# Optimization experiments

Measured on AMD Instinct MI355X. Metric: run time of the kernel, lower is better.

## Reference

```python
import jax, jax.numpy as jnp
import numpy as np

C_IN = 512
OUT_CH = 256  # query/key gate channels
DIM = 64      # squeeze/extraction rank


def setup_inputs() -> dict:
    key = jax.random.key(0)
    ks = jax.random.split(key, 11)
    b, c, h, w = 16, C_IN, 64, 64

    def winit(k, o, i):
        # torch Conv2d default init: U(-s, s), s = 1/sqrt(fan_in)
        s = 1.0 / np.sqrt(i)
        return jax.random.uniform(k, (o, i), jnp.float32, -s, s)

    return {
        "x": jax.random.normal(ks[0], (b, c, h, w), jnp.float32),
        "Wq": winit(ks[1], OUT_CH, C_IN), "bq": winit(ks[2], OUT_CH, C_IN)[:, 0],
        "Wk": winit(ks[3], OUT_CH, C_IN), "bk": winit(ks[4], OUT_CH, C_IN)[:, 0],
        "Wv": winit(ks[5], C_IN, C_IN),   "bv": winit(ks[6], C_IN, C_IN)[:, 0],
        "Ws": winit(ks[7], DIM, C_IN),    "bs": winit(ks[8], DIM, C_IN)[:, 0],
        "We": winit(ks[9], DIM, C_IN),    "be": winit(ks[10], DIM, C_IN)[:, 0],
    }


def reference(x, Wq, bq, Wk, bk, Wv, bv, Ws, bs, We, be):
    b, c, h, w = x.shape
    n = h * w
    xf = x.reshape(b, c, n)  # [b, 512, n] (1x1 conv == matmul over channels)

    Q = jnp.einsum('oc,bcn->bon', Wq, xf) + bq[:, None]   # [b, 256, n]
    K = jnp.einsum('oc,bcn->bon', Wk, xf) + bk[:, None]   # [b, 256, n]
    gate = jax.nn.sigmoid(jnp.mean(Q * K, axis=1, keepdims=True))  # [b, 1, n]

    V = jnp.einsum('oc,bcn->bon', Wv, xf) + bv[:, None]   # [b, 512, n]
    V_dw = V * gate                                        # [b, 512, n]

    Qs = jnp.einsum('oc,bcn->bon', Ws, xf) + bs[:, None]   # [b, 64, n]
    Ke = jnp.einsum('oc,bcn->bon', We, xf) + be[:, None]   # [b, 64, n]

    energy = jnp.einsum('bcn,bdn->bcd', V_dw, Qs)           # [b, 512, 64]
    attention = jax.nn.softmax(energy, axis=-1)
    Vout = jnp.einsum('bcd,bdn->bcn', attention, Ke)        # [b, 512, n]

    return x + Vout.reshape(b, c, h, w)
```

## Files before the change

### kernel.cpp

```cpp
#include <hip/hip_runtime.h>

#define BATCH 16
#define CIN 512
#define NPIX 4096

typedef __attribute__((ext_vector_type(8))) short bf16x8;
typedef __attribute__((ext_vector_type(4))) float f32x4;

#define MFMA(a,b,c) __builtin_amdgcn_mfma_f32_16x16x32_bf16((a),(b),(c),0,0,0)

#define GLOAD(g, l) __builtin_amdgcn_global_load_lds( \
    (const __attribute__((address_space(1))) unsigned int*)(g), \
    (__attribute__((address_space(3))) unsigned int*)(l), 16, 0, 0)

union PK  { short s[8]; bf16x8 v; };
union PK4 { short s[4]; uint2 u; };

__device__ __forceinline__ unsigned short bf16_rne(float f){
  unsigned u = __float_as_uint(f);
  return (unsigned short)((u + 0x7fffu + ((u >> 16) & 1u)) >> 16);
}
__device__ __forceinline__ void f32_split(float f, short &h, short &l){
  unsigned short hu = bf16_rne(f);
  h = (short)hu;
  float fh = __uint_as_float((unsigned)hu << 16);
  l = (short)bf16_rne(f - fh);
}
__device__ __forceinline__ void split8(float4 a, float4 b, bf16x8 &h, bf16x8 &l){
  float vv[8] = {a.x,a.y,a.z,a.w,b.x,b.y,b.z,b.w};
  PK ph, pl;
  #pragma unroll
  for (int z=0;z<8;z++){ short hh,ll; f32_split(vv[z],hh,ll); ph.s[z]=hh; pl.s[z]=ll; }
  h = ph.v; l = pl.v;
}

__device__ __forceinline__ int offBig(int row, int k){
  int s = k >> 3;
  s = (s & ~7) | ((s ^ row) & 7);
  return row*512 + s*8 + (k & 7);
}

__global__ __launch_bounds__(256)
void k_convw(const float* __restrict__ Wq, const float* __restrict__ bq,
             const float* __restrict__ Wk, const float* __restrict__ bk,
             const float* __restrict__ Ws, const float* __restrict__ bs,
             const float* __restrict__ We, const float* __restrict__ be,
             short* __restrict__ WALL, short* __restrict__ WLOT,
             float* __restrict__ BG, float* __restrict__ BSE){
  int t = blockIdx.x*256 + threadIdx.x;
  if (t < 640*512){
    int r = t >> 9, k = t & 511;
    float v = (r < 512) ? ((r & 1) ? Wk[(r>>1)*512 + k] : Wq[(r>>1)*512 + k])
            : (r < 576) ? Ws[(r-512)*512 + k] : We[(r-576)*512 + k];
    short h, l; f32_split(v, h, l);
    int kt = k >> 5, lc = (k >> 3) & 3, e = k & 7;
    int pc = lc ^ (r & 3);
    WALL[((size_t)kt*640 + r)*32 + pc*8 + e] = h;
    if (r >= 512 && r < 576){
      int rlo = r - 512;
      WLOT[((size_t)kt*64 + rlo)*32 + (lc ^ (rlo & 3))*8 + e] = l;
    }
  }
  if (t < 512) BG[t] = (t & 1) ? bk[t>>1] : bq[t>>1];
  if (t < 128) BSE[t] = (t < 64) ? bs[t] : be[t-64];
}

__global__ __launch_bounds__(512, 2)
void k_front(const float* __restrict__ x, const short* __restrict__ WALL,
             const short* __restrict__ WLOT, const float* __restrict__ BG,
             const float* __restrict__ BSE,
             float* __restrict__ QSG, short* __restrict__ KET, float* __restrict__ S){
  __shared__ __align__(16) short AB[2][640*32];
  __shared__ __align__(16) short LO[2][64*32];
  __shared__ __align__(16) short XS[64*512];
  __shared__ float QKf[512];
  __shared__ float GF[64];
  int nt = blockIdx.x, b = blockIdx.y;
  int n0 = nt*64;
  int tid = threadIdx.x, w = tid>>6, lane = tid&63;
  int lr = lane&15, lk = (lane>>4)<<3;
  int cg = lane>>4;

  {
    const char* src = (const char*)WALL;
    #pragma unroll
    for (int i=0;i<5;i++){
      int slot = i*8 + w;
      GLOAD(src + slot*1024 + lane*16, ((char*)&AB[0][0]) + slot*1024);
    }
    if (w < 4)
      GLOAD((const char*)WLOT + w*1024 + lane*16, ((char*)&LO[0][0]) + w*1024);
  }

  {
    int cc0 = tid >> 2;
    int ni  = (tid & 3) * 4;
    #pragma unroll
    for (int p=0;p<4;p++){
      int cc = p*128 + cc0;
      const float* xp = x + ((size_t)b*CIN + cc)*NPIX + n0 + ni;
      float4 vv[4];
      #pragma unroll
      for (int u=0;u<4;u++) vv[u] = *(const float4*)(xp + u*16);
      #pragma unroll
      for (int u=0;u<4;u++){
        float f[4] = {vv[u].x, vv[u].y, vv[u].z, vv[u].w};
        #pragma unroll
        for (int z=0;z<4;z++)
          XS[offBig(ni + u*16 + z, cc)] = (short)bf16_rne(f[z]);
      }
    }
  }

  f32x4 acc[5][4] = {};
  int rowBase = w*80;

  for (int kt=0; kt<16; kt++){
    int cur = kt & 1;
    __syncthreads();
    if (kt < 15){
      const char* src = (const char*)WALL + (size_t)(kt+1)*40960;
      #pragma unroll
      for (int i=0;i<5;i++){
        int slot = i*8 + w;
        GLOAD(src + slot*1024 + lane*16, ((char*)&AB[cur^1][0]) + slot*1024);
      }
      if (w < 4)
        GLOAD((const char*)WLOT + (size_t)(kt+1)*4096 + w*1024 + lane*16,
              ((char*)&LO[cur^1][0]) + w*1024);
    }
    bf16x8 bb[4];
    #pragma unroll
    for (int j=0;j<4;j++)
      bb[j] = *(const bf16x8*)&XS[offBig(j*16+lr, kt*32+lk)];
    int swz = ((cg ^ (lr & 3)) << 3);
    #pragma unroll
    for (int r=0;r<5;r++){
      int rowL = rowBase + r*16 + lr;
      bf16x8 a = *(const bf16x8*)&AB[cur][rowL*32 + swz];
      #pragma unroll
      for (int j=0;j<4;j++) acc[r][j] = MFMA(a, bb[j], acc[r][j]);
      int F = w*5 + r;
      if (F >= 32 && F < 36){
        int rowLo = F*16 - 512 + lr;
        bf16x8 alo = *(const bf16x8*)&LO[cur][rowLo*32 + swz];
        #pragma unroll
        for (int j=0;j<4;j++) acc[r][j] = MFMA(alo, bb[j], acc[r][j]);
      }
    }
  }

  int rq = (lane>>4)<<2;
  {
    float p[4] = {0.f,0.f,0.f,0.f};
    #pragma unroll
    for (int r=0;r<5;r++){
      int F = w*5 + r;
      if (F < 32){
        f32x4 bg = *(const f32x4*)&BG[F*16 + rq];
        #pragma unroll
        for (int j=0;j<4;j++){
          f32x4 a4 = acc[r][j];
          p[j] += (a4[0]+bg[0])*(a4[1]+bg[1]) + (a4[2]+bg[2])*(a4[3]+bg[3]);
        }
      }
    }
    #pragma unroll
    for (int j=0;j<4;j++){ p[j] += __shfl_xor(p[j],16); p[j] += __shfl_xor(p[j],32); }
    if (lane < 16){
      #pragma unroll
      for (int j=0;j<4;j++) QKf[w*64 + j*16 + lane] = p[j];
    }
  }
  __syncthreads();
  if (tid < 64){
    float s = 0.f;
    #pragma unroll
    for (int ww=0;ww<8;ww++) s += QKf[ww*64 + tid];
    GF[tid] = 1.f/(1.f + __expf(-s*(1.f/256.f)));
  }
  __syncthreads();

  #pragma unroll
  for (int r=0;r<5;r++){
    int F = w*5 + r;
    if (F >= 32 && F < 36){
      int row0 = F*16 - 512 + rq;
      f32x4 bs4 = *(const f32x4*)&BSE[row0];
      float srow[4] = {0.f,0.f,0.f,0.f};
      #pragma unroll
      for (int j=0;j<4;j++){
        int nl = j*16 + lr;
        float g = GF[nl];
        int n = n0 + nl;
        #pragma unroll
        for (int q=0;q<4;q++){
          float v = (acc[r][j][q] + bs4[q]) * g;
          QSG[((size_t)(b*64) + row0 + q)*NPIX + n] = v;
          srow[q] += v;
        }
      }
      #pragma unroll
      for (int q=0;q<4;q++){
        float v = srow[q];
        v += __shfl_xor(v,1); v += __shfl_xor(v,2);
        v += __shfl_xor(v,4); v += __shfl_xor(v,8);
        if (lr == 0) atomicAdd(&S[b*64 + row0 + q], v);
      }
    } else if (F >= 36){
      int d0 = F*16 - 576 + rq;
      f32x4 be4 = *(const f32x4*)&BSE[64 + d0];
      #pragma unroll
      for (int j=0;j<4;j++){
        int n = n0 + j*16 + lr;
        PK4 pk;
        #pragma unroll
        for (int q=0;q<4;q++) pk.s[q] = (short)bf16_rne(acc[r][j][q] + be4[q]);
        *(uint2*)&KET[((size_t)(b*NPIX) + n)*64 + d0] = pk.u;
      }
    }
  }
}

__global__ __launch_bounds__(512)
void k_M(const float* __restrict__ x, const float* __restrict__ QSG,
         float* __restrict__ M){
  int slab = blockIdx.x, b = blockIdx.y;
  int tid = threadIdx.x, w = tid>>6, lane = tid&63;
  int lr = lane&15, lk8 = (lane>>4)<<3;
  f32x4 acc[4][4] = {};
  for (int kt=0; kt<8; kt++){
    int noff = slab*256 + kt*32 + lk8;
    bf16x8 bh[4], bl[4];
    #pragma unroll
    for (int j=0;j<4;j++){
      const float* qp = QSG + ((size_t)(b*64) + j*16 + lr)*NPIX + noff;
      split8(*(const float4*)qp, *(const float4*)(qp+4), bh[j], bl[j]);
    }
    #pragma unroll
    for (int r=0;r<4;r++){
      const float* xp = x + ((size_t)(b*CIN) + w*64 + r*16 + lr)*NPIX + noff;
      bf16x8 ah, al;
      split8(*(const float4*)xp, *(const float4*)(xp+4), ah, al);
      #pragma unroll
      for (int j=0;j<4;j++){
        acc[r][j] = MFMA(al, bh[j], acc[r][j]);
        acc[r][j] = MFMA(ah, bl[j], acc[r][j]);
        acc[r][j] = MFMA(ah, bh[j], acc[r][j]);
      }
    }
  }
  int rq = (lane>>4)<<2;
  #pragma unroll
  for (int r=0;r<4;r++)
    #pragma unroll
    for (int j=0;j<4;j++)
      #pragma unroll
      for (int q=0;q<4;q++)
        atomicAdd(&M[((size_t)(b*CIN) + w*64 + r*16 + rq + q)*64 + j*16 + lr], acc[r][j][q]);
}

__global__ __launch_bounds__(256)
void k_energy(const float* __restrict__ Wv, const float* __restrict__ bv,
              const float* __restrict__ M, const float* __restrict__ S,
              float* __restrict__ EN){
  __shared__ __align__(16) float ML[128*68];
  int cch = blockIdx.x, b = blockIdx.y;
  int tid = threadIdx.x;
  int d4 = tid & 15, ci = tid >> 4;
  f32x4 acc[2] = {};
  for (int kt=0; kt<4; kt++){
    __syncthreads();
    for (int i = tid; i < 2048; i += 256){
      int k = i >> 4, c4 = (i & 15) * 4;
      *(float4*)&ML[k*68 + c4] = *(const float4*)&M[((size_t)(b*CIN) + kt*128 + k)*64 + c4];
    }
    __syncthreads();
    #pragma unroll
    for (int m=0;m<2;m++){
      int c = cch*32 + ci + 16*m;
      const float* wvp = Wv + (size_t)c*512 + kt*128;
      for (int k4=0;k4<32;k4++){
        float4 wv4 = *(const float4*)(wvp + k4*4);
        f32x4 m0 = *(const f32x4*)&ML[(k4*4+0)*68 + d4*4];
        f32x4 m1 = *(const f32x4*)&ML[(k4*4+1)*68 + d4*4];
        f32x4 m2 = *(const f32x4*)&ML[(k4*4+2)*68 + d4*4];
        f32x4 m3 = *(const f32x4*)&ML[(k4*4+3)*68 + d4*4];
        acc[m] += m0*wv4.x + m1*wv4.y + m2*wv4.z + m3*wv4.w;
      }
    }
  }
  f32x4 s4 = *(const f32x4*)&S[b*64 + d4*4];
  #pragma unroll
  for (int m=0;m<2;m++){
    int c = cch*32 + ci + 16*m;
    f32x4 r = acc[m] + s4*bv[c];
    *(f32x4*)&EN[((size_t)(b*CIN) + c)*64 + d4*4] = r;
  }
}

__global__ __launch_bounds__(256)
void k_softmax(const float* __restrict__ EN, short* __restrict__ ATT){
  int row = blockIdx.x*4 + (threadIdx.x>>6);
  int lane = threadIdx.x & 63;
  float v = EN[(size_t)row*64 + lane];
  float m = v;
  #pragma unroll
  for (int s=1;s<64;s<<=1) m = fmaxf(m, __shfl_xor(m, s));
  float e = __expf(v - m);
  float sum = e;
  #pragma unroll
  for (int s=1;s<64;s<<=1) sum += __shfl_xor(sum, s);
  ATT[(size_t)row*64 + lane] = (short)bf16_rne(e / sum);
}

__global__ __launch_bounds__(512)
void k_out(const float* __restrict__ x, const short* __restrict__ ATT,
           const short* __restrict__ KET, float* __restrict__ out){
  int nt = blockIdx.x, b = blockIdx.y;
  int n0 = nt*64;
  int tid = threadIdx.x, w = tid>>6, lane = tid&63;
  int lr = lane&15, lk = (lane>>4)<<3;
  f32x4 acc[4][4] = {};
  #pragma unroll
  for (int kt=0; kt<2; kt++){
    bf16x8 bb[4];
    #pragma unroll
    for (int j=0;j<4;j++)
      bb[j] = *(const bf16x8*)&KET[((size_t)(b*NPIX) + n0 + j*16 + lr)*64 + kt*32 + lk];
    #pragma unroll
    for (int r=0;r<4;r++){
      bf16x8 a = *(const bf16x8*)&ATT[((size_t)(b*CIN) + w*64 + r*16 + lr)*64 + kt*32 + lk];
      #pragma unroll
      for (int j=0;j<4;j++)
        acc[r][j] = MFMA(a, bb[j], acc[r][j]);
    }
  }
  int rq = (lane>>4)<<2;
  #pragma unroll
  for (int r=0;r<4;r++)
    #pragma unroll
    for (int j=0;j<4;j++){
      int col = n0 + j*16 + lr;
      #pragma unroll
      for (int q=0;q<4;q++){
        size_t idx = ((size_t)(b*CIN) + w*64 + r*16 + rq + q)*NPIX + col;
        out[idx] = x[idx] + acc[r][j][q];
      }
    }
}

extern "C" void kernel_launch(void* const* d_in, const int* in_sizes, int n_in,
                              void* d_out, int out_size, void* d_ws, size_t ws_size,
                              hipStream_t stream){
  const float* x   = (const float*)d_in[0];
  const float* Wq  = (const float*)d_in[1];
  const float* bq  = (const float*)d_in[2];
  const float* Wk  = (const float*)d_in[3];
  const float* bk  = (const float*)d_in[4];
  const float* Wv  = (const float*)d_in[5];
  const float* bv  = (const float*)d_in[6];
  const float* Wsq = (const float*)d_in[7];
  const float* bsq = (const float*)d_in[8];
  const float* We  = (const float*)d_in[9];
  const float* be  = (const float*)d_in[10];
  float* out = (float*)d_out;

  char* wsb = (char*)d_ws;
  size_t off = 0;
  auto alloc = [&](size_t bytes)->void*{
    void* p = wsb + off; off += (bytes + 255) & ~(size_t)255; return p;
  };
  short* WALL = (short*)alloc((size_t)640*512*2);
  short* WLOT = (short*)alloc((size_t)64*512*2);
  float* BG   = (float*)alloc(512*4);
  float* BSE  = (float*)alloc(128*4);
  float* QSG  = (float*)alloc((size_t)BATCH*64*NPIX*4);
  short* KET  = (short*)alloc((size_t)BATCH*NPIX*64*2);
  float* Mb   = (float*)alloc((size_t)BATCH*512*64*4);
  float* Sb   = (float*)alloc((size_t)BATCH*64*4);
  float* EN   = (float*)alloc((size_t)BATCH*512*64*4);
  short* ATT  = (short*)alloc((size_t)BATCH*512*64*2);

  hipMemsetAsync(Mb, 0, (size_t)BATCH*512*64*4, stream);
  hipMemsetAsync(Sb, 0, (size_t)BATCH*64*4, stream);

  k_convw  <<<1280, 256, 0, stream>>>(Wq,bq,Wk,bk,Wsq,bsq,We,be, WALL,WLOT,BG,BSE);
  k_front  <<<dim3(64,16), 512, 0, stream>>>(x, WALL, WLOT, BG, BSE, QSG, KET, Sb);
  k_M      <<<dim3(16,16), 512, 0, stream>>>(x, QSG, Mb);
  k_energy <<<dim3(16,16), 256, 0, stream>>>(Wv, bv, Mb, Sb, EN);
  k_softmax<<<2048, 256, 0, stream>>>(EN, ATT);
  k_out    <<<dim3(64,16), 512, 0, stream>>>(x, ATT, KET, out);
}
```

Before: 276.0 us.

## Double k_front pixel tile and read weights straight from global memory

The front projection kernel now processes 128 pixels per block instead of 64, which halves the grid and doubles the per-wave accumulators to 5x8 MFMA tiles. This reuses each weight fragment across twice as many pixels. The double-buffered LDS staging of the weight tiles through global_load_lds is removed, and the A fragments are loaded directly from global memory each k-step. In exchange, weight-load latency is no longer hidden by prefetch, register pressure roughly doubles with a risk of spills, and the 128 KB activation tile in LDS limits the kernel to one block per CU.

```diff
diff --git a/kernel.cpp b/kernel.cpp
--- a/kernel.cpp
+++ b/kernel.cpp
@@ -8,10 +8,6 @@
 typedef __attribute__((ext_vector_type(4))) float f32x4;
 
 #define MFMA(a,b,c) __builtin_amdgcn_mfma_f32_16x16x32_bf16((a),(b),(c),0,0,0)
-
-#define GLOAD(g, l) __builtin_amdgcn_global_load_lds( \
-    (const __attribute__((address_space(1))) unsigned int*)(g), \
-    (__attribute__((address_space(3))) unsigned int*)(l), 16, 0, 0)
 
 union PK  { short s[8]; bf16x8 v; };
 union PK4 { short s[4]; uint2 u; };
@@ -70,40 +66,27 @@
              const short* __restrict__ WLOT, const float* __restrict__ BG,
              const float* __restrict__ BSE,
              float* __restrict__ QSG, short* __restrict__ KET, float* __restrict__ S){
-  __shared__ __align__(16) short AB[2][640*32];
-  __shared__ __align__(16) short LO[2][64*32];
-  __shared__ __align__(16) short XS[64*512];
-  __shared__ float QKf[512];
-  __shared__ float GF[64];
+  __shared__ __align__(16) short XS[128*512];
+  __shared__ float QKf[8*128];
+  __shared__ float GF[128];
   int nt = blockIdx.x, b = blockIdx.y;
-  int n0 = nt*64;
+  int n0 = nt*128;
   int tid = threadIdx.x, w = tid>>6, lane = tid&63;
   int lr = lane&15, lk = (lane>>4)<<3;
   int cg = lane>>4;
 
   {
-    const char* src = (const char*)WALL;
-    #pragma unroll
-    for (int i=0;i<5;i++){
-      int slot = i*8 + w;
-      GLOAD(src + slot*1024 + lane*16, ((char*)&AB[0][0]) + slot*1024);
-    }
-    if (w < 4)
-      GLOAD((const char*)WLOT + w*1024 + lane*16, ((char*)&LO[0][0]) + w*1024);
-  }
-
-  {
-    int cc0 = tid >> 2;
-    int ni  = (tid & 3) * 4;
+    int c0 = tid >> 2;
+    int ni = (tid & 3) * 4;
     #pragma unroll
     for (int p=0;p<4;p++){
-      int cc = p*128 + cc0;
+      int cc = p*128 + c0;
       const float* xp = x + ((size_t)b*CIN + cc)*NPIX + n0 + ni;
-      float4 vv[4];
-      #pragma unroll
-      for (int u=0;u<4;u++) vv[u] = *(const float4*)(xp + u*16);
-      #pragma unroll
-      for (int u=0;u<4;u++){
+      float4 vv[8];
+      #pragma unroll
+      for (int u=0;u<8;u++) vv[u] = *(const float4*)(xp + u*16);
+      #pragma unroll
+      for (int u=0;u<8;u++){
         float f[4] = {vv[u].x, vv[u].y, vv[u].z, vv[u].w};
         #pragma unroll
         for (int z=0;z<4;z++)
@@ -111,72 +94,60 @@
       }
     }
   }
-
-  f32x4 acc[5][4] = {};
+  __syncthreads();
+
+  f32x4 acc[5][8] = {};
   int rowBase = w*80;
+  int swz = ((cg ^ (lr & 3)) << 3);
 
   for (int kt=0; kt<16; kt++){
-    int cur = kt & 1;
-    __syncthreads();
-    if (kt < 15){
-      const char* src = (const char*)WALL + (size_t)(kt+1)*40960;
-      #pragma unroll
-      for (int i=0;i<5;i++){
-        int slot = i*8 + w;
-        GLOAD(src + slot*1024 + lane*16, ((char*)&AB[cur^1][0]) + slot*1024);
-      }
-      if (w < 4)
-        GLOAD((const char*)WLOT + (size_t)(kt+1)*4096 + w*1024 + lane*16,
-              ((char*)&LO[cur^1][0]) + w*1024);
-    }
-    bf16x8 bb[4];
-    #pragma unroll
-    for (int j=0;j<4;j++)
+    bf16x8 bb[8];
+    #pragma unroll
+    for (int j=0;j<8;j++)
       bb[j] = *(const bf16x8*)&XS[offBig(j*16+lr, kt*32+lk)];
-    int swz = ((cg ^ (lr & 3)) << 3);
+    const short* wk = WALL + (size_t)kt*640*32;
     #pragma unroll
     for (int r=0;r<5;r++){
       int rowL = rowBase + r*16 + lr;
-      bf16x8 a = *(const bf16x8*)&AB[cur][rowL*32 + swz];
-      #pragma unroll
-      for (int j=0;j<4;j++) acc[r][j] = MFMA(a, bb[j], acc[r][j]);
+      bf16x8 a = *(const bf16x8*)&wk[rowL*32 + swz];
+      #pragma unroll
+      for (int j=0;j<8;j++) acc[r][j] = MFMA(a, bb[j], acc[r][j]);
       int F = w*5 + r;
       if (F >= 32 && F < 36){
-        int rowLo = F*16 - 512 + lr;
-        bf16x8 alo = *(const bf16x8*)&LO[cur][rowLo*32 + swz];
-        #pragma unroll
-        for (int j=0;j<4;j++) acc[r][j] = MFMA(alo, bb[j], acc[r][j]);
+        bf16x8 alo = *(const bf16x8*)&WLOT[(size_t)kt*64*32 + (F*16-512+lr)*32 + swz];
+        #pragma unroll
+        for (int j=0;j<8;j++) acc[r][j] = MFMA(alo, bb[j], acc[r][j]);
       }
     }
   }
 
   int rq = (lane>>4)<<2;
   {
-    float p[4] = {0.f,0.f,0.f,0.f};
+    float p[8] = {0.f,0.f,0.f,0.f,0.f,0.f,0.f,0.f};
     #pragma unroll
     for (int r=0;r<5;r++){
       int F = w*5 + r;
       if (F < 32){
         f32x4 bg = *(const f32x4*)&BG[F*16 + rq];
         #pragma unroll
-        for (int j=0;j<4;j++){
+        for (int j=0;j<8;j++){
           f32x4 a4 = acc[r][j];
           p[j] += (a4[0]+bg[0])*(a4[1]+bg[1]) + (a4[2]+bg[2])*(a4[3]+bg[3]);
         }
       }
     }
     #pragma unroll
-    for (int j=0;j<4;j++){ p[j] += __shfl_xor(p[j],16); p[j] += __shfl_xor(p[j],32); }
+    for (int j=0;j<8;j++){ p[j] += __shfl_xor(p[j],16); p[j] += __shfl_xor(p[j],32); }
     if (lane < 16){
       #pragma unroll
-      for (int j=0;j<4;j++) QKf[w*64 + j*16 + lane] = p[j];
+      for (int j=0;j<8;j++) QKf[w*128 + j*16 + lane] = p[j];
     }
   }
   __syncthreads();
-  if (tid < 64){
+  if (tid < 128){
     float s = 0.f;
     #pragma unroll
-    for (int ww=0;ww<8;ww++) s += QKf[ww*64 + tid];
+    for (int ww=0;ww<8;ww++) s += QKf[ww*128 + tid];
     GF[tid] = 1.f/(1.f + __expf(-s*(1.f/256.f)));
   }
   __syncthreads();
@@ -189,7 +160,7 @@
       f32x4 bs4 = *(const f32x4*)&BSE[row0];
       float srow[4] = {0.f,0.f,0.f,0.f};
       #pragma unroll
-      for (int j=0;j<4;j++){
+      for (int j=0;j<8;j++){
         int nl = j*16 + lr;
         float g = GF[nl];
         int n = n0 + nl;
@@ -211,7 +182,7 @@
       int d0 = F*16 - 576 + rq;
       f32x4 be4 = *(const f32x4*)&BSE[64 + d0];
       #pragma unroll
-      for (int j=0;j<4;j++){
+      for (int j=0;j<8;j++){
         int n = n0 + j*16 + lr;
         PK4 pk;
         #pragma unroll
@@ -386,7 +357,7 @@
   hipMemsetAsync(Sb, 0, (size_t)BATCH*64*4, stream);
 
   k_convw  <<<1280, 256, 0, stream>>>(Wq,bq,Wk,bk,Wsq,bsq,We,be, WALL,WLOT,BG,BSE);
-  k_front  <<<dim3(64,16), 512, 0, stream>>>(x, WALL, WLOT, BG, BSE, QSG, KET, Sb);
+  k_front  <<<dim3(32,16), 512, 0, stream>>>(x, WALL, WLOT, BG, BSE, QSG, KET, Sb);
   k_M      <<<dim3(16,16), 512, 0, stream>>>(x, QSG, Mb);
   k_energy <<<dim3(16,16), 256, 0, stream>>>(Wv, bv, Mb, Sb, EN);
   k_softmax<<<2048, 256, 0, stream>>>(EN, ATT);
```

New measurement: 266.1 us. -3.6%, faster.
